# Kernel tuning notes

Hardware: AMD Instinct MI355X
Metric: run time of the kernel (lower is better)

## Reference

```python
import jax, jax.numpy as jnp
import numpy as np

N_USER, N_ITEM, D = 50000, 100000, 64
E_UI, E_UU = 1000000, 800000
NEG_SLOPE = 0.2


def gatv2(x_src, x_dst, src_idx, dst_idx, w_src, w_dst, attn, bias, n_dst):
    """DGL GATv2Conv, num_heads=1: e = a . leaky_relu(Ws x_u + Wd x_v),
    segment-softmax over edges incoming to each dst node, message = Ws x_u."""
    hs = x_src @ w_src                      # [Ns, D]
    hd = x_dst @ w_dst                      # [Nd, D]
    pre = jax.nn.leaky_relu(hs[src_idx] + hd[dst_idx], NEG_SLOPE)  # [E, D]
    e = pre @ attn                          # [E]
    emax = jax.ops.segment_max(e, dst_idx, num_segments=n_dst)     # -inf for empty
    a = jnp.exp(e - emax[dst_idx])          # [E]
    denom = jax.ops.segment_sum(a, dst_idx, num_segments=n_dst)    # [Nd]
    num = jax.ops.segment_sum(hs[src_idx] * a[:, None], dst_idx, num_segments=n_dst)
    out = num / jnp.maximum(denom, 1e-9)[:, None]
    return out + bias


def setup_inputs() -> dict:
    key = jax.random.key(0)
    ks = jax.random.split(key, 32)
    s = 1.0 / np.sqrt(D)
    def W(k):
        return jax.random.normal(k, (D, D), jnp.float32) * s
    inp = {
        "h_user": jax.random.normal(ks[0], (N_USER, D), jnp.float32),
        "h_item": jax.random.normal(ks[1], (N_ITEM, D), jnp.float32),
        "rate_src": jax.random.randint(ks[2], (E_UI,), 0, N_USER, jnp.int32),
        "rate_dst": jax.random.randint(ks[3], (E_UI,), 0, N_ITEM, jnp.int32),
        "rb_src": jax.random.randint(ks[4], (E_UI,), 0, N_ITEM, jnp.int32),
        "rb_dst": jax.random.randint(ks[5], (E_UI,), 0, N_USER, jnp.int32),
        "link_src": jax.random.randint(ks[6], (E_UU,), 0, N_USER, jnp.int32),
        "link_dst": jax.random.randint(ks[7], (E_UU,), 0, N_USER, jnp.int32),
    }
    names = ["r1", "rb1", "rb2", "l2"]
    for i, nm in enumerate(names):
        inp[f"w_src_{nm}"] = W(ks[8 + 4 * i])
        inp[f"w_dst_{nm}"] = W(ks[9 + 4 * i])
        inp[f"a_{nm}"] = jax.random.normal(ks[10 + 4 * i], (D,), jnp.float32) * s
        inp[f"b_{nm}"] = jnp.zeros((D,), jnp.float32)
    inp["w_out"] = jax.random.normal(ks[24], (2 * D, D), jnp.float32) * (1.0 / np.sqrt(2 * D))
    inp["b_out"] = jnp.zeros((D,), jnp.float32)
    return inp


def reference(h_user, h_item,
              w_src_r1, w_dst_r1, a_r1, b_r1,
              w_src_rb1, w_dst_rb1, a_rb1, b_rb1,
              w_src_rb2, w_dst_rb2, a_rb2, b_rb2,
              w_src_l2, w_dst_l2, a_l2, b_l2,
              w_out, b_out,
              rate_src, rate_dst, rb_src, rb_dst, link_src, link_dst):
    # layer1 'rate': user -> item
    h1_item = gatv2(h_user, h_item, rate_src, rate_dst,
                    w_src_r1, w_dst_r1, a_r1, b_r1, N_ITEM)
    # layer1 'rated-by': item -> user
    h2_user = gatv2(h_item, h_user, rb_src, rb_dst,
                    w_src_rb1, w_dst_rb1, a_rb1, b_rb1, N_USER)
    # layer2 'rated-by': item(h1) -> user
    infl_user = gatv2(h1_item, h_user, rb_src, rb_dst,
                      w_src_rb2, w_dst_rb2, a_rb2, b_rb2, N_USER)
    # layer2 'link': user(h2) -> user
    social_user = gatv2(h2_user, h_user, link_src, link_dst,
                        w_src_l2, w_dst_l2, a_l2, b_l2, N_USER)
    out = jnp.concatenate([infl_user, social_user], axis=1) @ w_out + b_out
    return out
```

## Files before the change

kernel.cpp:

```cpp
#include <hip/hip_runtime.h>
#include <hip/hip_fp16.h>
#include <math.h>

#define N_USER 50000
#define N_ITEM 100000
#define E_UI   1000000
#define E_UU   800000
#define E_TOT  (E_UI + E_UI + E_UU)
#define NEG_SLOPE 0.2f
#define LOG2E 1.4426950408889634f

#define NB0 391
#define NB1 196
#define NB2 196
#define NBTOT (NB0 + NB1 + NB2)
#define GPB 256
#define MATN (NBTOT * 256)
#define NBP  ((MATN + 1023) / 1024)

#define XS_STRIDE 68

typedef _Float16 h2v __attribute__((ext_vector_type(2)));

#if defined(__has_builtin)
#if __has_builtin(__builtin_amdgcn_fdot2)
#define HAS_FDOT2 1
#endif
#if __has_builtin(__builtin_elementwise_max)
#define HAS_EW_MAX 1
#endif
#if __has_builtin(__builtin_amdgcn_exp2f)
#define HAS_EXP2 1
#endif
#endif

__device__ __forceinline__ float fexp2(float x) {
#ifdef HAS_EXP2
  return __builtin_amdgcn_exp2f(x);
#else
  return exp2f(x);
#endif
}

__device__ __forceinline__ float fdot2acc(__half2 a, __half2 b, float c) {
#ifdef HAS_FDOT2
  return __builtin_amdgcn_fdot2(__builtin_bit_cast(h2v, a), __builtin_bit_cast(h2v, b), c, false);
#else
  float2 af = __half22float2(a), bf = __half22float2(b);
  return fmaf(af.x, bf.x, fmaf(af.y, bf.y, c));
#endif
}

__device__ __forceinline__ __half2 h2max(__half2 a, __half2 b) {
  h2v av = __builtin_bit_cast(h2v, a), bv = __builtin_bit_cast(h2v, b);
#ifdef HAS_EW_MAX
  h2v r = __builtin_elementwise_max(av, bv);
#else
  h2v r; r.x = av.x > bv.x ? av.x : bv.x; r.y = av.y > bv.y ? av.y : bv.y;
#endif
  return __builtin_bit_cast(__half2, r);
}

__device__ __forceinline__ __half2 h2min(__half2 a, __half2 b) {
  h2v av = __builtin_bit_cast(h2v, a), bv = __builtin_bit_cast(h2v, b);
#ifdef HAS_EW_MAX
  h2v r = __builtin_elementwise_min(av, bv);
#else
  h2v r; r.x = av.x < bv.x ? av.x : bv.x; r.y = av.y < bv.y ? av.y : bv.y;
#endif
  return __builtin_bit_cast(__half2, r);
}


__global__ __launch_bounds__(256) void bucket_hist(const int* __restrict__ d0, const int* __restrict__ d1,
                                                   const int* __restrict__ d2, int* __restrict__ mat) {
  int gid = blockIdx.x >> 8;
  int g   = blockIdx.x & 255;
  const int* dst = gid == 0 ? d0 : (gid == 1 ? d1 : d2);
  int E    = (gid == 2) ? E_UU : E_UI;
  int NB   = (gid == 0) ? NB0 : NB1;
  int boff = (gid == 0) ? 0 : (gid == 1 ? NB0 : NB0 + NB1);
  __shared__ int cnt[NB0];
  for (int b = threadIdx.x; b < NB; b += 256) cnt[b] = 0;
  __syncthreads();
  int chunk = (E + 255) >> 8;
  int lo = g * chunk, hi = min(lo + chunk, E);
  for (int i = lo + threadIdx.x; i < hi; i += 256)
    atomicAdd(&cnt[dst[i] >> 8], 1);
  __syncthreads();
  for (int b = threadIdx.x; b < NB; b += 256)
    mat[(boff + b) * 256 + g] = cnt[b];
}


__global__ __launch_bounds__(256) void partial_kernel(const int* __restrict__ counts, int n,
                                                      int* __restrict__ partials) {
  int t = threadIdx.x;
  int base = blockIdx.x * 1024 + t * 4;
  int s = 0;
  if (base + 3 < n) {
    int4 v = *(const int4*)(counts + base);
    s = v.x + v.y + v.z + v.w;
  } else {
    for (int i = base; i < n && i < base + 4; ++i) s += counts[i];
  }
  #pragma unroll
  for (int off = 1; off < 64; off <<= 1) s += __shfl_xor(s, off);
  __shared__ int ws[4];
  if ((t & 63) == 0) ws[t >> 6] = s;
  __syncthreads();
  if (t == 0) partials[blockIdx.x] = ws[0] + ws[1] + ws[2] + ws[3];
}

__global__ __launch_bounds__(256) void scan_apply_fused(const int* __restrict__ counts, int n,
                                                        const int* __restrict__ partials, int nbp,
                                                        int* __restrict__ outp) {
  __shared__ int sp[256];
  int t = threadIdx.x;
  sp[t] = (t < nbp) ? partials[t] : 0;
  __syncthreads();
  for (int off = 1; off < 256; off <<= 1) {
    int v = (t >= off) ? sp[t - off] : 0;
    __syncthreads();
    sp[t] += v;
    __syncthreads();
  }
  int block_off = (blockIdx.x == 0) ? 0 : sp[blockIdx.x - 1];

  int base = blockIdx.x * 1024 + t * 4;
  int4 v = make_int4(0, 0, 0, 0);
  if (base + 3 < n) {
    v = *(const int4*)(counts + base);
  } else {
    int* pv = &v.x;
    for (int i = 0; i < 4; ++i) if (base + i < n) pv[i] = counts[base + i];
  }
  int s = v.x + v.y + v.z + v.w;
  int lane = t & 63;
  int wv = t >> 6;
  int inc = s;
  #pragma unroll
  for (int off = 1; off < 64; off <<= 1) {
    int u = __shfl_up(inc, off);
    if (lane >= off) inc += u;
  }
  __shared__ int wsum[4];
  if (lane == 63) wsum[wv] = inc;
  __syncthreads();
  int woff = 0;
  for (int i = 0; i < wv; ++i) woff += wsum[i];
  int excl = woff + (inc - s) + block_off;
  int4 rp;
  rp.x = excl;
  rp.y = rp.x + v.x;
  rp.z = rp.y + v.y;
  rp.w = rp.z + v.z;
  if (base + 3 < n) {
    *(int4*)(outp + base) = rp;
  } else {
    int* pr = &rp.x;
    for (int i = 0; i < 4; ++i) if (base + i < n) outp[base + i] = pr[i];
  }
}


__global__ __launch_bounds__(256) void bucket_scatter(const int* __restrict__ s0v, const int* __restrict__ d0,
                                                      const int* __restrict__ s1v, const int* __restrict__ d1,
                                                      const int* __restrict__ s2v, const int* __restrict__ d2,
                                                      const int* __restrict__ mscan, unsigned int* __restrict__ pairs) {
  int gid = blockIdx.x >> 8;
  int g   = blockIdx.x & 255;
  const int* src = gid == 0 ? s0v : (gid == 1 ? s1v : s2v);
  const int* dst = gid == 0 ? d0  : (gid == 1 ? d1  : d2);
  int E    = (gid == 2) ? E_UU : E_UI;
  int NB   = (gid == 0) ? NB0 : NB1;
  int boff = (gid == 0) ? 0 : (gid == 1 ? NB0 : NB0 + NB1);
  __shared__ int cur[NB0];
  for (int b = threadIdx.x; b < NB; b += 256) cur[b] = mscan[(boff + b) * 256 + g];
  __syncthreads();
  int chunk = (E + 255) >> 8;
  int lo = g * chunk, hi = min(lo + chunk, E);
  for (int i = lo + threadIdx.x; i < hi; i += 256) {
    int d = dst[i], s = src[i];
    int pos = atomicAdd(&cur[d >> 8], 1);
    pairs[pos] = ((unsigned)(d & 255) << 24) | (unsigned)s;
  }
}


__global__ __launch_bounds__(256) void bucket_finalize(const unsigned int* __restrict__ pairs,
                                                       const int* __restrict__ mscan,
                                                       int* __restrict__ rp, int* __restrict__ col) {
  int gb = blockIdx.x;
  int t  = threadIdx.x;
  int gid  = (gb < NB0) ? 0 : (gb < NB0 + NB1 ? 1 : 2);
  int boff = (gid == 0) ? 0 : (gid == 1 ? NB0 : NB0 + NB1);
  int node_goff = (gid == 0) ? 0 : (gid == 1 ? N_ITEM : N_ITEM + N_USER);
  int n    = (gid == 0) ? N_ITEM : N_USER;
  int b_local = gb - boff;
  int bs = mscan[gb * 256];
  int be = (gb + 1 < NBTOT) ? mscan[(gb + 1) * 256] : E_TOT;

  __shared__ int cnt[256];
  __shared__ int curb[256];
  __shared__ int wsum[4];
  cnt[t] = 0;
  __syncthreads();
  for (int i = bs + t; i < be; i += 256)
    atomicAdd(&cnt[pairs[i] >> 24], 1);
  __syncthreads();

  int v = cnt[t];
  int lane = t & 63, wv = t >> 6;
  int inc = v;
  #pragma unroll
  for (int off = 1; off < 64; off <<= 1) {
    int u = __shfl_up(inc, off);
    if (lane >= off) inc += u;
  }
  if (lane == 63) wsum[wv] = inc;
  __syncthreads();
  int woff = 0;
  for (int i = 0; i < wv; ++i) woff += wsum[i];
  int base = bs + woff + (inc - v);

  int node_local = b_local * 256 + t;
  if (node_local < n) rp[node_goff + node_local] = base;
  if (gb == NBTOT - 1 && t == 255) rp[N_ITEM + 2 * N_USER] = E_TOT;
  curb[t] = base;
  __syncthreads();

  for (int i = bs + t; i < be; i += 256) {
    unsigned u = pairs[i];
    int p = atomicAdd(&curb[u >> 24], 1);
    col[p] = (int)(u & 0xFFFFFFu);
  }
}


__device__ __forceinline__ void load_xtile(const float* __restrict__ X, float* Xs, int base, int N) {
  #pragma unroll
  for (int i = 0; i < 4; ++i) {
    int idx = threadIdx.x * 4 + i * 1024;
    int row = idx >> 6, colc = idx & 63;
    int grow = base + row;
    const float* src = X + (size_t)(grow < N ? grow : N - 1) * 64 + colc;
    *(float4*)(Xs + row * XS_STRIDE + colc) = *(const float4*)src;
  }
}

__device__ __forceinline__ void gemm_phase(const float* __restrict__ Wsrc, float* Ws,
                                           const float* x0, const float* x1,
                                           const float* x2, const float* x3, int c4,
                                           float4& acc0, float4& acc1, float4& acc2, float4& acc3) {
  __syncthreads();
  #pragma unroll
  for (int i = 0; i < 4; ++i) {
    int idx = threadIdx.x * 4 + i * 1024;
    *(float4*)(Ws + idx) = *(const float4*)(Wsrc + idx);
  }
  __syncthreads();
  acc0 = make_float4(0.f, 0.f, 0.f, 0.f);
  acc1 = acc0; acc2 = acc0; acc3 = acc0;
  #pragma unroll 4
  for (int k4 = 0; k4 < 64; k4 += 4) {
    float4 xa = *(const float4*)(x0 + k4);
    float4 xb = *(const float4*)(x1 + k4);
    float4 xc = *(const float4*)(x2 + k4);
    float4 xd = *(const float4*)(x3 + k4);
    #pragma unroll
    for (int kk = 0; kk < 4; ++kk) {
      float4 w = *(const float4*)(Ws + (k4 + kk) * 64 + c4);
      float sa = (&xa.x)[kk], sb = (&xb.x)[kk], sc = (&xc.x)[kk], sd = (&xd.x)[kk];
      acc0.x = fmaf(sa, w.x, acc0.x); acc0.y = fmaf(sa, w.y, acc0.y);
      acc0.z = fmaf(sa, w.z, acc0.z); acc0.w = fmaf(sa, w.w, acc0.w);
      acc1.x = fmaf(sb, w.x, acc1.x); acc1.y = fmaf(sb, w.y, acc1.y);
      acc1.z = fmaf(sb, w.z, acc1.z); acc1.w = fmaf(sb, w.w, acc1.w);
      acc2.x = fmaf(sc, w.x, acc2.x); acc2.y = fmaf(sc, w.y, acc2.y);
      acc2.z = fmaf(sc, w.z, acc2.z); acc2.w = fmaf(sc, w.w, acc2.w);
      acc3.x = fmaf(sd, w.x, acc3.x); acc3.y = fmaf(sd, w.y, acc3.y);
      acc3.z = fmaf(sd, w.z, acc3.z); acc3.w = fmaf(sd, w.w, acc3.w);
    }
  }
}

__device__ __forceinline__ void store4_f32(float* __restrict__ Y, int r0, int r1, int r2, int r3,
                                           int N, int c4,
                                           const float4& a0, const float4& a1,
                                           const float4& a2, const float4& a3) {
  if (r0 < N) *(float4*)(Y + (size_t)r0 * 64 + c4) = a0;
  if (r1 < N) *(float4*)(Y + (size_t)r1 * 64 + c4) = a1;
  if (r2 < N) *(float4*)(Y + (size_t)r2 * 64 + c4) = a2;
  if (r3 < N) *(float4*)(Y + (size_t)r3 * 64 + c4) = a3;
}

__device__ __forceinline__ void store4_f16(__half* __restrict__ Y, int r0, int r1, int r2, int r3,
                                           int N, int c4,
                                           const float4& a0, const float4& a1,
                                           const float4& a2, const float4& a3) {
  uint2 st;
  if (r0 < N) {
    st.x = __builtin_bit_cast(unsigned int, __floats2half2_rn(a0.x, a0.y));
    st.y = __builtin_bit_cast(unsigned int, __floats2half2_rn(a0.z, a0.w));
    *(uint2*)(Y + (size_t)r0 * 64 + c4) = st;
  }
  if (r1 < N) {
    st.x = __builtin_bit_cast(unsigned int, __floats2half2_rn(a1.x, a1.y));
    st.y = __builtin_bit_cast(unsigned int, __floats2half2_rn(a1.z, a1.w));
    *(uint2*)(Y + (size_t)r1 * 64 + c4) = st;
  }
  if (r2 < N) {
    st.x = __builtin_bit_cast(unsigned int, __floats2half2_rn(a2.x, a2.y));
    st.y = __builtin_bit_cast(unsigned int, __floats2half2_rn(a2.z, a2.w));
    *(uint2*)(Y + (size_t)r2 * 64 + c4) = st;
  }
  if (r3 < N) {
    st.x = __builtin_bit_cast(unsigned int, __floats2half2_rn(a3.x, a3.y));
    st.y = __builtin_bit_cast(unsigned int, __floats2half2_rn(a3.z, a3.w));
    *(uint2*)(Y + (size_t)r3 * 64 + c4) = st;
  }
}

__global__ __launch_bounds__(256) void gemm_user4(const float* __restrict__ X,
                                                  const float* __restrict__ W0, const float* __restrict__ W1,
                                                  const float* __restrict__ W2, const float* __restrict__ W3,
                                                  __half* __restrict__ Y0h, float* __restrict__ Y1,
                                                  float* __restrict__ Y2, float* __restrict__ Y3, int N) {
  __shared__ float Xs[64 * XS_STRIDE];
  __shared__ float Ws[64 * 64];
  int base = blockIdx.x * 64;
  load_xtile(X, Xs, base, N);
  int c4 = (threadIdx.x & 15) * 4;
  int rl = threadIdx.x >> 4;
  int r0 = base + rl, r1 = r0 + 16, r2 = r0 + 32, r3 = r0 + 48;
  const float* x0 = Xs + (rl +  0) * XS_STRIDE;
  const float* x1 = Xs + (rl + 16) * XS_STRIDE;
  const float* x2 = Xs + (rl + 32) * XS_STRIDE;
  const float* x3 = Xs + (rl + 48) * XS_STRIDE;
  float4 a0, a1, a2, a3;
  gemm_phase(W0, Ws, x0, x1, x2, x3, c4, a0, a1, a2, a3);
  store4_f16(Y0h, r0, r1, r2, r3, N, c4, a0, a1, a2, a3);
  gemm_phase(W1, Ws, x0, x1, x2, x3, c4, a0, a1, a2, a3);
  store4_f32(Y1, r0, r1, r2, r3, N, c4, a0, a1, a2, a3);
  gemm_phase(W2, Ws, x0, x1, x2, x3, c4, a0, a1, a2, a3);
  store4_f32(Y2, r0, r1, r2, r3, N, c4, a0, a1, a2, a3);
  gemm_phase(W3, Ws, x0, x1, x2, x3, c4, a0, a1, a2, a3);
  store4_f32(Y3, r0, r1, r2, r3, N, c4, a0, a1, a2, a3);
}

__global__ __launch_bounds__(256) void gemm_item2(const float* __restrict__ X,
                                                  const float* __restrict__ W0, const float* __restrict__ W1,
                                                  float* __restrict__ Y0, __half* __restrict__ Y1h, int N) {
  __shared__ float Xs[64 * XS_STRIDE];
  __shared__ float Ws[64 * 64];
  int base = blockIdx.x * 64;
  load_xtile(X, Xs, base, N);
  int c4 = (threadIdx.x & 15) * 4;
  int rl = threadIdx.x >> 4;
  int r0 = base + rl, r1 = r0 + 16, r2 = r0 + 32, r3 = r0 + 48;
  const float* x0 = Xs + (rl +  0) * XS_STRIDE;
  const float* x1 = Xs + (rl + 16) * XS_STRIDE;
  const float* x2 = Xs + (rl + 32) * XS_STRIDE;
  const float* x3 = Xs + (rl + 48) * XS_STRIDE;
  float4 a0, a1, a2, a3;
  gemm_phase(W0, Ws, x0, x1, x2, x3, c4, a0, a1, a2, a3);
  store4_f32(Y0, r0, r1, r2, r3, N, c4, a0, a1, a2, a3);
  gemm_phase(W1, Ws, x0, x1, x2, x3, c4, a0, a1, a2, a3);
  store4_f16(Y1h, r0, r1, r2, r3, N, c4, a0, a1, a2, a3);
}

__global__ __launch_bounds__(256) void gemm_mid2x(const float* __restrict__ XA, const float* __restrict__ WA,
                                                  __half* __restrict__ YA, int NA, int nbA,
                                                  const float* __restrict__ XB, const float* __restrict__ WB,
                                                  __half* __restrict__ YB, int NB_) {
  __shared__ float Ws[64 * 64];
  const float* X; const float* W; __half* Y; int N; int base;
  if ((int)blockIdx.x < nbA) {
    X = XA; W = WA; Y = YA; N = NA; base = blockIdx.x * 64;
  } else {
    X = XB; W = WB; Y = YB; N = NB_; base = (blockIdx.x - nbA) * 64;
  }
  int c4 = (threadIdx.x & 15) * 4;
  int rl = threadIdx.x >> 4;
  int r0 = base + rl, r1 = r0 + 16, r2 = r0 + 32, r3 = r0 + 48;
  const float* x0 = X + (size_t)(r0 < N ? r0 : N - 1) * 64;
  const float* x1 = X + (size_t)(r1 < N ? r1 : N - 1) * 64;
  const float* x2 = X + (size_t)(r2 < N ? r2 : N - 1) * 64;
  const float* x3 = X + (size_t)(r3 < N ? r3 : N - 1) * 64;
  float4 a0, a1, a2, a3;
  gemm_phase(W, Ws, x0, x1, x2, x3, c4, a0, a1, a2, a3);
  store4_f16(Y, r0, r1, r2, r3, N, c4, a0, a1, a2, a3);
}


__global__ __launch_bounds__(256) void gat4n_kernel(
    const __half* __restrict__ hsA, const float* __restrict__ hdAp,
    const int* __restrict__ rpA, const float* __restrict__ attnA, const float* __restrict__ biasA,
    float* __restrict__ outA, int NdA,
    const __half* __restrict__ hsB, const float* __restrict__ hdBp,
    const int* __restrict__ rpB, const float* __restrict__ attnB, const float* __restrict__ biasB,
    float* __restrict__ outB, int NdB,
    const int* __restrict__ col) {
  int w = (blockIdx.x * blockDim.x + threadIdx.x) >> 6;
  int g = (threadIdx.x >> 4) & 3;
  int sl = threadIdx.x & 15;
  int node = w * 4 + g;
  bool valid = node < NdA + NdB;
  bool inA = node < NdA;
  const __half* hs  = inA ? hsA  : hsB;
  const float* hd   = inA ? hdAp : hdBp;
  const int* rp     = inA ? rpA  : rpB;
  const float* attn = inA ? attnA : attnB;
  const float* bias = inA ? biasA : biasB;
  float* outp       = inA ? outA : outB;
  int nn = inA ? node : node - NdA;
  if (!valid) nn = 0;
  int s0 = valid ? rp[nn] : 0;
  int s1 = valid ? rp[nn + 1] : 0;

  float4 hdf = valid ? *(const float4*)(hd + (size_t)nn * 64 + sl * 4) : make_float4(0.f, 0.f, 0.f, 0.f);
  float4 af  = *(const float4*)(attn + sl * 4);
  __half2 hd2a = __floats2half2_rn(hdf.x, hdf.y);
  __half2 hd2b = __floats2half2_rn(hdf.z, hdf.w);
  __half2 a2a = __floats2half2_rn(af.x * LOG2E, af.y * LOG2E);
  __half2 a2b = __floats2half2_rn(af.z * LOG2E, af.w * LOG2E);
  const __half2 C02 = __floats2half2_rn(NEG_SLOPE, NEG_SLOPE);
  const __half2 Z   = __floats2half2_rn(0.f, 0.f);

  float m = -1e30f, den = 0.f;
  float n0 = 0.f, n1 = 0.f, n2 = 0.f, n3 = 0.f;

  for (int e = s0; e < s1; e += 4) {
    int e1 = e + 1, e2 = e + 2, e3 = e + 3;
    bool h1 = e1 < s1, h2c = e2 < s1, h3 = e3 < s1;
    int sa = col[e];
    int sb = col[h1 ? e1 : e];
    int sc = col[h2c ? e2 : e];
    int sd = col[h3 ? e3 : e];
    uint2 ra = *(const uint2*)(hs + (size_t)sa * 64 + sl * 4);
    uint2 rb = *(const uint2*)(hs + (size_t)sb * 64 + sl * 4);
    uint2 rc = *(const uint2*)(hs + (size_t)sc * 64 + sl * 4);
    uint2 rd = *(const uint2*)(hs + (size_t)sd * 64 + sl * 4);

    __half2 xa0 = __hadd2(__builtin_bit_cast(__half2, ra.x), hd2a);
    __half2 xa1 = __hadd2(__builtin_bit_cast(__half2, ra.y), hd2b);
    __half2 xb0 = __hadd2(__builtin_bit_cast(__half2, rb.x), hd2a);
    __half2 xb1 = __hadd2(__builtin_bit_cast(__half2, rb.y), hd2b);
    __half2 xc0 = __hadd2(__builtin_bit_cast(__half2, rc.x), hd2a);
    __half2 xc1 = __hadd2(__builtin_bit_cast(__half2, rc.y), hd2b);
    __half2 xd0 = __hadd2(__builtin_bit_cast(__half2, rd.x), hd2a);
    __half2 xd1 = __hadd2(__builtin_bit_cast(__half2, rd.y), hd2b);
    __half2 la0 = __hfma2(C02, h2min(xa0, Z), h2max(xa0, Z));
    __half2 la1 = __hfma2(C02, h2min(xa1, Z), h2max(xa1, Z));
    __half2 lb0 = __hfma2(C02, h2min(xb0, Z), h2max(xb0, Z));
    __half2 lb1 = __hfma2(C02, h2min(xb1, Z), h2max(xb1, Z));
    __half2 lc0 = __hfma2(C02, h2min(xc0, Z), h2max(xc0, Z));
    __half2 lc1 = __hfma2(C02, h2min(xc1, Z), h2max(xc1, Z));
    __half2 ld0 = __hfma2(C02, h2min(xd0, Z), h2max(xd0, Z));
    __half2 ld1 = __hfma2(C02, h2min(xd1, Z), h2max(xd1, Z));
    float ta = fdot2acc(a2b, la1, fdot2acc(a2a, la0, 0.f));
    float tb = fdot2acc(a2b, lb1, fdot2acc(a2a, lb0, 0.f));
    float tc = fdot2acc(a2b, lc1, fdot2acc(a2a, lc0, 0.f));
    float td = fdot2acc(a2b, ld1, fdot2acc(a2a, ld0, 0.f));
    #pragma unroll
    for (int off = 1; off < 16; off <<= 1) {
      ta += __shfl_xor(ta, off);
      tb += __shfl_xor(tb, off);
      tc += __shfl_xor(tc, off);
      td += __shfl_xor(td, off);
    }
    if (!h1)  tb = -1e30f;
    if (!h2c) tc = -1e30f;
    if (!h3)  td = -1e30f;

    float tp = fmaxf(fmaxf(ta, tb), fmaxf(tc, td));
    float dd = tp - m;
    if (dd > 11.5f) {
      float sc0 = fexp2(-dd);
      den *= sc0; n0 *= sc0; n1 *= sc0; n2 *= sc0; n3 *= sc0;
      m = tp;
    }
    float pa = fexp2(ta - m);
    float pb = fexp2(tb - m);
    float pc = fexp2(tc - m);
    float pd = fexp2(td - m);
    den += (pa + pb) + (pc + pd);
    __half2 pab = __floats2half2_rn(pa, pb);
    __half2 pcd = __floats2half2_rn(pc, pd);

    unsigned lo_ab_x = (ra.x & 0xFFFFu) | (rb.x << 16);
    unsigned hi_ab_x = (ra.x >> 16) | (rb.x & 0xFFFF0000u);
    unsigned lo_ab_y = (ra.y & 0xFFFFu) | (rb.y << 16);
    unsigned hi_ab_y = (ra.y >> 16) | (rb.y & 0xFFFF0000u);
    unsigned lo_cd_x = (rc.x & 0xFFFFu) | (rd.x << 16);
    unsigned hi_cd_x = (rc.x >> 16) | (rd.x & 0xFFFF0000u);
    unsigned lo_cd_y = (rc.y & 0xFFFFu) | (rd.y << 16);
    unsigned hi_cd_y = (rc.y >> 16) | (rd.y & 0xFFFF0000u);

    n0 = fdot2acc(pcd, __builtin_bit_cast(__half2, lo_cd_x),
         fdot2acc(pab, __builtin_bit_cast(__half2, lo_ab_x), n0));
    n1 = fdot2acc(pcd, __builtin_bit_cast(__half2, hi_cd_x),
         fdot2acc(pab, __builtin_bit_cast(__half2, hi_ab_x), n1));
    n2 = fdot2acc(pcd, __builtin_bit_cast(__half2, lo_cd_y),
         fdot2acc(pab, __builtin_bit_cast(__half2, lo_ab_y), n2));
    n3 = fdot2acc(pcd, __builtin_bit_cast(__half2, hi_cd_y),
         fdot2acc(pab, __builtin_bit_cast(__half2, hi_ab_y), n3));
  }

  if (valid) {
    float inv = 1.f / fmaxf(den, 1e-9f);
    float4 b4 = *(const float4*)(bias + sl * 4);
    float4 o;
    o.x = fmaf(n0, inv, b4.x);
    o.y = fmaf(n1, inv, b4.y);
    o.z = fmaf(n2, inv, b4.z);
    o.w = fmaf(n3, inv, b4.w);
    *(float4*)(outp + (size_t)nn * 64 + sl * 4) = o;
  }
}


__global__ __launch_bounds__(256) void final_kernel(const float* __restrict__ A, const float* __restrict__ B,
                                                    const float* __restrict__ W, const float* __restrict__ bias,
                                                    float* __restrict__ Y, int N) {
  __shared__ float Ws[128 * 64];
  #pragma unroll
  for (int i = 0; i < 8; ++i) {
    int idx = threadIdx.x * 4 + i * 1024;
    *(float4*)(Ws + idx) = *(const float4*)(W + idx);
  }
  __syncthreads();
  int c4 = (threadIdx.x & 15) * 4;
  int rl = threadIdx.x >> 4;
  int base = blockIdx.x * 64;

  float4 b4 = *(const float4*)(bias + c4);

  #pragma unroll
  for (int rr = 0; rr < 4; ++rr) {
    int row = base + rr * 16 + rl;
    if (row >= N) continue;
    const float* ar = A + (size_t)row * 64;
    const float* br = B + (size_t)row * 64;
    float4 acc = b4;
    #pragma unroll 4
    for (int k4 = 0; k4 < 64; k4 += 4) {
      float4 xa = *(const float4*)(ar + k4);
      float4 xb = *(const float4*)(br + k4);
      #pragma unroll
      for (int kk = 0; kk < 4; ++kk) {
        float4 wa = *(const float4*)(Ws + (k4 + kk) * 64 + c4);
        float4 wb = *(const float4*)(Ws + (64 + k4 + kk) * 64 + c4);
        float xsa = (&xa.x)[kk], xsb = (&xb.x)[kk];
        acc.x = fmaf(xsa, wa.x, acc.x); acc.x = fmaf(xsb, wb.x, acc.x);
        acc.y = fmaf(xsa, wa.y, acc.y); acc.y = fmaf(xsb, wb.y, acc.y);
        acc.z = fmaf(xsa, wa.z, acc.z); acc.z = fmaf(xsb, wb.z, acc.z);
        acc.w = fmaf(xsa, wa.w, acc.w); acc.w = fmaf(xsb, wb.w, acc.w);
      }
    }
    *(float4*)(Y + (size_t)row * 64 + c4) = acc;
  }
}


extern "C" void kernel_launch(void* const* d_in, const int* in_sizes, int n_in,
                              void* d_out, int out_size, void* d_ws, size_t ws_size,
                              hipStream_t stream) {
  const float* h_user   = (const float*)d_in[0];
  const float* h_item   = (const float*)d_in[1];
  const int* rate_src   = (const int*)d_in[2];
  const int* rate_dst   = (const int*)d_in[3];
  const int* rb_src     = (const int*)d_in[4];
  const int* rb_dst     = (const int*)d_in[5];
  const int* link_src   = (const int*)d_in[6];
  const int* link_dst   = (const int*)d_in[7];
  const float* w_src_r1  = (const float*)d_in[8];
  const float* w_dst_r1  = (const float*)d_in[9];
  const float* a_r1      = (const float*)d_in[10];
  const float* b_r1      = (const float*)d_in[11];
  const float* w_src_rb1 = (const float*)d_in[12];
  const float* w_dst_rb1 = (const float*)d_in[13];
  const float* a_rb1     = (const float*)d_in[14];
  const float* b_rb1     = (const float*)d_in[15];
  const float* w_src_rb2 = (const float*)d_in[16];
  const float* w_dst_rb2 = (const float*)d_in[17];
  const float* a_rb2     = (const float*)d_in[18];
  const float* b_rb2     = (const float*)d_in[19];
  const float* w_src_l2  = (const float*)d_in[20];
  const float* w_dst_l2  = (const float*)d_in[21];
  const float* a_l2      = (const float*)d_in[22];
  const float* b_l2      = (const float*)d_in[23];
  const float* w_out     = (const float*)d_in[24];
  const float* b_out     = (const float*)d_in[25];
  float* out = (float*)d_out;

  char* ws = (char*)d_ws;
  size_t off = 0;
  auto alloc = [&](size_t bytes) -> void* {
    void* p = ws + off;
    off += (bytes + 255) & ~(size_t)255;
    return p;
  };

  float* u1 = (float*)alloc((size_t)N_USER * 64 * 4);
  float* u2 = (float*)alloc((size_t)N_USER * 64 * 4);
  float* u3 = (float*)alloc((size_t)N_USER * 64 * 4);
  float* i0 = (float*)alloc((size_t)N_ITEM * 64 * 4);
  __half* uh0 = (__half*)alloc((size_t)N_USER * 64 * 2);
  __half* ih1 = (__half*)alloc((size_t)N_ITEM * 64 * 2);

  int* mat     = (int*)alloc((size_t)MATN * 4);
  int* mscan   = (int*)alloc((size_t)MATN * 4);
  int* partials= (int*)alloc(256 * 4);
  int* grp     = (int*)alloc((size_t)(N_ITEM + 2 * N_USER + 1) * 4);
  unsigned int* pairs = (unsigned int*)alloc((size_t)E_TOT * 4);
  int* col_all = (int*)alloc((size_t)E_TOT * 4);

  bucket_hist<<<3 * GPB, 256, 0, stream>>>(rate_dst, rb_dst, link_dst, mat);
  partial_kernel<<<NBP, 256, 0, stream>>>(mat, MATN, partials);
  scan_apply_fused<<<NBP, 256, 0, stream>>>(mat, MATN, partials, NBP, mscan);
  bucket_scatter<<<3 * GPB, 256, 0, stream>>>(rate_src, rate_dst, rb_src, rb_dst,
                                              link_src, link_dst, mscan, pairs);
  bucket_finalize<<<NBTOT, 256, 0, stream>>>(pairs, mscan, grp, col_all);

  int* rp_rate = grp;
  int* rp_rb   = grp + N_ITEM;
  int* rp_link = grp + N_ITEM + N_USER;

  gemm_user4<<<(N_USER + 63) / 64, 256, 0, stream>>>(
      h_user, w_src_r1, w_dst_rb1, w_dst_rb2, w_dst_l2, uh0, u1, u2, u3, N_USER);
  gemm_item2<<<(N_ITEM + 63) / 64, 256, 0, stream>>>(
      h_item, w_dst_r1, w_src_rb1, i0, ih1, N_ITEM);

  {
    int nodes = N_ITEM + N_USER;
    int waves = (nodes + 3) / 4;
    gat4n_kernel<<<(waves + 3) / 4, 256, 0, stream>>>(
        uh0, i0, rp_rate, a_r1,  b_r1,  i0, N_ITEM,
        ih1, u1, rp_rb,   a_rb1, b_rb1, u1, N_USER,
        col_all);
  }

  {
    int nbA = (N_ITEM + 63) / 64;
    int nbB = (N_USER + 63) / 64;
    gemm_mid2x<<<nbA + nbB, 256, 0, stream>>>(
        i0, w_src_rb2, ih1, N_ITEM, nbA,
        u1, w_src_l2,  uh0, N_USER);
  }

  {
    int nodes = N_USER + N_USER;
    int waves = (nodes + 3) / 4;
    gat4n_kernel<<<(waves + 3) / 4, 256, 0, stream>>>(
        ih1, u2, rp_rb,   a_rb2, b_rb2, u2, N_USER,
        uh0, u3, rp_link, a_l2,  b_l2,  u3, N_USER,
        col_all);
  }

  final_kernel<<<(N_USER + 63) / 64, 256, 0, stream>>>(u2, u3, w_out, b_out, out, N_USER);
}
```

Baseline: 274.2 us.

## Process 16 destination nodes per wave with 4 lanes per node

```diff
diff --git a/kernel.cpp b/kernel.cpp
--- a/kernel.cpp
+++ b/kernel.cpp
@@ -393,7 +393,7 @@
 }
 
 
-__global__ __launch_bounds__(256) void gat4n_kernel(
+__global__ __launch_bounds__(256) void gat16n_kernel(
     const __half* __restrict__ hsA, const float* __restrict__ hdAp,
     const int* __restrict__ rpA, const float* __restrict__ attnA, const float* __restrict__ biasA,
     float* __restrict__ outA, int NdA,
@@ -402,9 +402,9 @@
     float* __restrict__ outB, int NdB,
     const int* __restrict__ col) {
   int w = (blockIdx.x * blockDim.x + threadIdx.x) >> 6;
-  int g = (threadIdx.x >> 4) & 3;
-  int sl = threadIdx.x & 15;
-  int node = w * 4 + g;
+  int grp = (threadIdx.x >> 2) & 15;
+  int q   = threadIdx.x & 3;
+  int node = w * 16 + grp;
   bool valid = node < NdA + NdB;
   bool inA = node < NdA;
   const __half* hs  = inA ? hsA  : hsB;
@@ -418,104 +418,96 @@
   int s0 = valid ? rp[nn] : 0;
   int s1 = valid ? rp[nn + 1] : 0;
 
-  float4 hdf = valid ? *(const float4*)(hd + (size_t)nn * 64 + sl * 4) : make_float4(0.f, 0.f, 0.f, 0.f);
-  float4 af  = *(const float4*)(attn + sl * 4);
-  __half2 hd2a = __floats2half2_rn(hdf.x, hdf.y);
-  __half2 hd2b = __floats2half2_rn(hdf.z, hdf.w);
-  __half2 a2a = __floats2half2_rn(af.x * LOG2E, af.y * LOG2E);
-  __half2 a2b = __floats2half2_rn(af.z * LOG2E, af.w * LOG2E);
   const __half2 C02 = __floats2half2_rn(NEG_SLOPE, NEG_SLOPE);
   const __half2 Z   = __floats2half2_rn(0.f, 0.f);
 
+  __half2 hd2[8], a2[8];
+  {
+    const float* hp = hd + (size_t)nn * 64 + q * 16;
+    #pragma unroll
+    for (int i = 0; i < 4; ++i) {
+      float4 v = *(const float4*)(hp + i * 4);
+      hd2[2 * i]     = __floats2half2_rn(v.x, v.y);
+      hd2[2 * i + 1] = __floats2half2_rn(v.z, v.w);
+    }
+    const float* ap = attn + q * 16;
+    #pragma unroll
+    for (int i = 0; i < 4; ++i) {
+      float4 v = *(const float4*)(ap + i * 4);
+      a2[2 * i]     = __floats2half2_rn(v.x * LOG2E, v.y * LOG2E);
+      a2[2 * i + 1] = __floats2half2_rn(v.z * LOG2E, v.w * LOG2E);
+    }
+  }
+
   float m = -1e30f, den = 0.f;
-  float n0 = 0.f, n1 = 0.f, n2 = 0.f, n3 = 0.f;
-
-  for (int e = s0; e < s1; e += 4) {
-    int e1 = e + 1, e2 = e + 2, e3 = e + 3;
-    bool h1 = e1 < s1, h2c = e2 < s1, h3 = e3 < s1;
+  float num[16];
+  #pragma unroll
+  for (int i = 0; i < 16; ++i) num[i] = 0.f;
+
+  for (int e = s0; e < s1; e += 2) {
+    bool h1 = (e + 1) < s1;
     int sa = col[e];
-    int sb = col[h1 ? e1 : e];
-    int sc = col[h2c ? e2 : e];
-    int sd = col[h3 ? e3 : e];
-    uint2 ra = *(const uint2*)(hs + (size_t)sa * 64 + sl * 4);
-    uint2 rb = *(const uint2*)(hs + (size_t)sb * 64 + sl * 4);
-    uint2 rc = *(const uint2*)(hs + (size_t)sc * 64 + sl * 4);
-    uint2 rd = *(const uint2*)(hs + (size_t)sd * 64 + sl * 4);
-
-    __half2 xa0 = __hadd2(__builtin_bit_cast(__half2, ra.x), hd2a);
-    __half2 xa1 = __hadd2(__builtin_bit_cast(__half2, ra.y), hd2b);
-    __half2 xb0 = __hadd2(__builtin_bit_cast(__half2, rb.x), hd2a);
-    __half2 xb1 = __hadd2(__builtin_bit_cast(__half2, rb.y), hd2b);
-    __half2 xc0 = __hadd2(__builtin_bit_cast(__half2, rc.x), hd2a);
-    __half2 xc1 = __hadd2(__builtin_bit_cast(__half2, rc.y), hd2b);
-    __half2 xd0 = __hadd2(__builtin_bit_cast(__half2, rd.x), hd2a);
-    __half2 xd1 = __hadd2(__builtin_bit_cast(__half2, rd.y), hd2b);
-    __half2 la0 = __hfma2(C02, h2min(xa0, Z), h2max(xa0, Z));
-    __half2 la1 = __hfma2(C02, h2min(xa1, Z), h2max(xa1, Z));
-    __half2 lb0 = __hfma2(C02, h2min(xb0, Z), h2max(xb0, Z));
-    __half2 lb1 = __hfma2(C02, h2min(xb1, Z), h2max(xb1, Z));
-    __half2 lc0 = __hfma2(C02, h2min(xc0, Z), h2max(xc0, Z));
-    __half2 lc1 = __hfma2(C02, h2min(xc1, Z), h2max(xc1, Z));
-    __half2 ld0 = __hfma2(C02, h2min(xd0, Z), h2max(xd0, Z));
-    __half2 ld1 = __hfma2(C02, h2min(xd1, Z), h2max(xd1, Z));
-    float ta = fdot2acc(a2b, la1, fdot2acc(a2a, la0, 0.f));
-    float tb = fdot2acc(a2b, lb1, fdot2acc(a2a, lb0, 0.f));
-    float tc = fdot2acc(a2b, lc1, fdot2acc(a2a, lc0, 0.f));
-    float td = fdot2acc(a2b, ld1, fdot2acc(a2a, ld0, 0.f));
+    int sb = col[h1 ? e + 1 : e];
+    const __half* pra = hs + (size_t)sa * 64 + q * 16;
+    const __half* prb = hs + (size_t)sb * 64 + q * 16;
+    uint4 ra0 = *(const uint4*)(pra);
+    uint4 ra1 = *(const uint4*)(pra + 8);
+    uint4 rb0 = *(const uint4*)(prb);
+    uint4 rb1 = *(const uint4*)(prb + 8);
+    unsigned rau[8] = {ra0.x, ra0.y, ra0.z, ra0.w, ra1.x, ra1.y, ra1.z, ra1.w};
+    unsigned rbu[8] = {rb0.x, rb0.y, rb0.z, rb0.w, rb1.x, rb1.y, rb1.z, rb1.w};
+
+    float ta = 0.f, tb = 0.f;
     #pragma unroll
-    for (int off = 1; off < 16; off <<= 1) {
-      ta += __shfl_xor(ta, off);
-      tb += __shfl_xor(tb, off);
-      tc += __shfl_xor(tc, off);
-      td += __shfl_xor(td, off);
-    }
-    if (!h1)  tb = -1e30f;
-    if (!h2c) tc = -1e30f;
-    if (!h3)  td = -1e30f;
-
-    float tp = fmaxf(fmaxf(ta, tb), fmaxf(tc, td));
+    for (int i = 0; i < 8; ++i) {
+      __half2 xa = __hadd2(__builtin_bit_cast(__half2, rau[i]), hd2[i]);
+      __half2 la = __hfma2(C02, h2min(xa, Z), h2max(xa, Z));
+      ta = fdot2acc(a2[i], la, ta);
+      __half2 xb = __hadd2(__builtin_bit_cast(__half2, rbu[i]), hd2[i]);
+      __half2 lb = __hfma2(C02, h2min(xb, Z), h2max(xb, Z));
+      tb = fdot2acc(a2[i], lb, tb);
+    }
+    ta += __shfl_xor(ta, 1); ta += __shfl_xor(ta, 2);
+    tb += __shfl_xor(tb, 1); tb += __shfl_xor(tb, 2);
+    if (!h1) tb = -1e30f;
+
+    float tp = fmaxf(ta, tb);
     float dd = tp - m;
     if (dd > 11.5f) {
       float sc0 = fexp2(-dd);
-      den *= sc0; n0 *= sc0; n1 *= sc0; n2 *= sc0; n3 *= sc0;
+      den *= sc0;
+      #pragma unroll
+      for (int i = 0; i < 16; ++i) num[i] *= sc0;
       m = tp;
     }
     float pa = fexp2(ta - m);
     float pb = fexp2(tb - m);
-    float pc = fexp2(tc - m);
-    float pd = fexp2(td - m);
-    den += (pa + pb) + (pc + pd);
+    den += pa + pb;
     __half2 pab = __floats2half2_rn(pa, pb);
-    __half2 pcd = __floats2half2_rn(pc, pd);
-
-    unsigned lo_ab_x = (ra.x & 0xFFFFu) | (rb.x << 16);
-    unsigned hi_ab_x = (ra.x >> 16) | (rb.x & 0xFFFF0000u);
-    unsigned lo_ab_y = (ra.y & 0xFFFFu) | (rb.y << 16);
-    unsigned hi_ab_y = (ra.y >> 16) | (rb.y & 0xFFFF0000u);
-    unsigned lo_cd_x = (rc.x & 0xFFFFu) | (rd.x << 16);
-    unsigned hi_cd_x = (rc.x >> 16) | (rd.x & 0xFFFF0000u);
-    unsigned lo_cd_y = (rc.y & 0xFFFFu) | (rd.y << 16);
-    unsigned hi_cd_y = (rc.y >> 16) | (rd.y & 0xFFFF0000u);
-
-    n0 = fdot2acc(pcd, __builtin_bit_cast(__half2, lo_cd_x),
-         fdot2acc(pab, __builtin_bit_cast(__half2, lo_ab_x), n0));
-    n1 = fdot2acc(pcd, __builtin_bit_cast(__half2, hi_cd_x),
-         fdot2acc(pab, __builtin_bit_cast(__half2, hi_ab_x), n1));
-    n2 = fdot2acc(pcd, __builtin_bit_cast(__half2, lo_cd_y),
-         fdot2acc(pab, __builtin_bit_cast(__half2, lo_ab_y), n2));
-    n3 = fdot2acc(pcd, __builtin_bit_cast(__half2, hi_cd_y),
-         fdot2acc(pab, __builtin_bit_cast(__half2, hi_ab_y), n3));
+
+    #pragma unroll
+    for (int i = 0; i < 8; ++i) {
+      unsigned lo = (rau[i] & 0xFFFFu) | (rbu[i] << 16);
+      unsigned hi = (rau[i] >> 16) | (rbu[i] & 0xFFFF0000u);
+      num[2 * i]     = fdot2acc(__builtin_bit_cast(__half2, lo), pab, num[2 * i]);
+      num[2 * i + 1] = fdot2acc(__builtin_bit_cast(__half2, hi), pab, num[2 * i + 1]);
+    }
   }
 
   if (valid) {
     float inv = 1.f / fmaxf(den, 1e-9f);
-    float4 b4 = *(const float4*)(bias + sl * 4);
-    float4 o;
-    o.x = fmaf(n0, inv, b4.x);
-    o.y = fmaf(n1, inv, b4.y);
-    o.z = fmaf(n2, inv, b4.z);
-    o.w = fmaf(n3, inv, b4.w);
-    *(float4*)(outp + (size_t)nn * 64 + sl * 4) = o;
+    const float* bp = bias + q * 16;
+    float* op = outp + (size_t)nn * 64 + q * 16;
+    #pragma unroll
+    for (int i = 0; i < 4; ++i) {
+      float4 b4 = *(const float4*)(bp + i * 4);
+      float4 o;
+      o.x = fmaf(num[4 * i + 0], inv, b4.x);
+      o.y = fmaf(num[4 * i + 1], inv, b4.y);
+      o.z = fmaf(num[4 * i + 2], inv, b4.z);
+      o.w = fmaf(num[4 * i + 3], inv, b4.w);
+      *(float4*)(op + i * 4) = o;
+    }
   }
 }
 
@@ -634,8 +626,7 @@
 
   {
     int nodes = N_ITEM + N_USER;
-    int waves = (nodes + 3) / 4;
-    gat4n_kernel<<<(waves + 3) / 4, 256, 0, stream>>>(
+    gat16n_kernel<<<(nodes + 63) / 64, 256, 0, stream>>>(
         uh0, i0, rp_rate, a_r1,  b_r1,  i0, N_ITEM,
         ih1, u1, rp_rb,   a_rb1, b_rb1, u1, N_USER,
         col_all);
@@ -651,8 +642,7 @@
 
   {
     int nodes = N_USER + N_USER;
-    int waves = (nodes + 3) / 4;
-    gat4n_kernel<<<(waves + 3) / 4, 256, 0, stream>>>(
+    gat16n_kernel<<<(nodes + 63) / 64, 256, 0, stream>>>(
         ih1, u2, rp_rb,   a_rb2, b_rb2, u2, N_USER,
         uh0, u3, rp_link, a_l2,  b_l2,  u3, N_USER,
         col_all);
```

New measurement: 277.7 us. No clear change (+1.3%).
